# Kernel optimization log

Measured on AMD Instinct MI355X. Metric: run time of the kernel, lower is better.

Reference implementation:

```python
import jax, jax.numpy as jnp
import numpy as np

N_NODES = 100000
N_EDGES = 1600000
D_IN = 128
D_OUT = 128


def setup_inputs() -> dict:
    key = jax.random.key(0)
    ks = jax.random.split(key, 7)
    stdv = 1.0 / np.sqrt(D_OUT)
    x = jax.random.normal(ks[0], (N_NODES, D_IN), dtype=jnp.float32)
    W = jax.random.normal(ks[1], (D_IN, D_OUT), dtype=jnp.float32) * stdv
    lin_bias = jax.random.uniform(ks[2], (D_OUT,), minval=-stdv, maxval=stdv, dtype=jnp.float32)
    bias = jax.random.uniform(ks[3], (D_OUT,), minval=-stdv, maxval=stdv, dtype=jnp.float32)
    adj_rows = jax.random.randint(ks[4], (N_EDGES,), 0, N_NODES, dtype=jnp.int32)
    adj_cols = jax.random.randint(ks[5], (N_EDGES,), 0, N_NODES, dtype=jnp.int32)
    adj_vals = jax.random.uniform(ks[6], (N_EDGES,), dtype=jnp.float32)
    return {"x": x, "W": W, "lin_bias": lin_bias, "bias": bias,
            "adj_rows": adj_rows, "adj_cols": adj_cols, "adj_vals": adj_vals}


def reference(x, W, lin_bias, bias, adj_rows, adj_cols, adj_vals):
    # support = Linear(x)  -> [N, D_OUT]
    support = x @ W + lin_bias
    # out = spmm(adj, support): out[r] = sum_e vals[e] * support[cols[e]] for rows[e]==r
    msgs = adj_vals[:, None] * support[adj_cols]            # [E, D_OUT]
    out = jax.ops.segment_sum(msgs, adj_rows, num_segments=N_NODES)
    return out + bias
```

## Files before the change

### kernel.cpp

```cpp
#include <hip/hip_runtime.h>
#include <hip/hip_bf16.h>

#define N_NODES 100000
#define N_EDGES 1600000
#define D 128

#define NBLK 256
#define EPB (N_EDGES / NBLK)
#define BROWS 128
#define NB 782
#define PCAP 2816

typedef __attribute__((ext_vector_type(8))) short short8;
typedef __attribute__((ext_vector_type(4))) float f32x4;

__device__ inline unsigned short f2bf(float f) {
  union { float f; unsigned u; } c; c.f = f;
  const unsigned u = c.u;
  return (unsigned short)((u + 0x7FFF + ((u >> 16) & 1)) >> 16);
}
__device__ inline float bflo(unsigned u) { return __int_as_float(u << 16); }
__device__ inline float bfhi(unsigned u) { return __int_as_float(u & 0xFFFF0000u); }

__global__ __launch_bounds__(256) void prep_kernel(
    const float* __restrict__ W, unsigned short* __restrict__ Wt,
    int* __restrict__ gcur) {
  const int b = blockIdx.x;
  if (b < 16) {
    const int t = b * 256 + threadIdx.x;
    const int k = t >> 5, n4 = (t & 31) * 4;
    const float4 w = *(const float4*)(W + k * D + n4);
    Wt[(n4 + 0) * D + k] = f2bf(w.x);
    Wt[(n4 + 1) * D + k] = f2bf(w.y);
    Wt[(n4 + 2) * D + k] = f2bf(w.z);
    Wt[(n4 + 3) * D + k] = f2bf(w.w);
  } else {
    for (int i = threadIdx.x; i < NB; i += 256) gcur[i] = 0;
  }
}

#define GR 128
#define LDK 136
__global__ __launch_bounds__(256) void fused_kernel(
    const float* __restrict__ x, const unsigned short* __restrict__ Wt,
    const float* __restrict__ lin_bias, unsigned short* __restrict__ support,
    const int* __restrict__ rows, const int* __restrict__ cols,
    const float* __restrict__ vals, int* __restrict__ gcur,
    unsigned* __restrict__ pairs, unsigned char* __restrict__ rowlo) {
  __shared__ __align__(16) char smem[GR * LDK * 2];

  if (blockIdx.x < NBLK) {
    int* cnt = (int*)smem;
    int* cur = cnt + NB;
    const int t = threadIdx.x, blk = blockIdx.x;
    for (int i = t; i < NB; i += 256) cnt[i] = 0;
    __syncthreads();
    const int base = blk * EPB;
    for (int i = t; i < EPB; i += 256)
      atomicAdd(&cnt[rows[base + i] >> 7], 1);
    __syncthreads();
    for (int b = t; b < NB; b += 256) {
      const int c = cnt[b];
      cur[b] = c ? atomicAdd(&gcur[b], c) : 0;
    }
    __syncthreads();
    for (int i = t; i < EPB; i += 256) {
      const int e = base + i;
      const int r = rows[e];
      const int b = r >> 7;
      const int pos = atomicAdd(&cur[b], 1);
      if (pos < PCAP) {
        const unsigned q = (unsigned)(vals[e] * 32767.f + 0.5f);
        pairs[(size_t)b * PCAP + pos] = ((unsigned)cols[e] << 15) | q;
        rowlo[(size_t)b * PCAP + pos] = (unsigned char)(r & (BROWS - 1));
      }
    }
    return;
  }

  unsigned short* xb = (unsigned short*)smem;
  const int t = threadIdx.x;
  const int row0 = (blockIdx.x - NBLK) * GR;

  for (int i = t; i < GR * 32; i += 256) {
    const int r = i >> 5, k4 = (i & 31) * 4;
    const int row = row0 + r;
    float4 v = make_float4(0.f, 0.f, 0.f, 0.f);
    if (row < N_NODES) v = *(const float4*)(x + (size_t)row * D + k4);
    unsigned short* p = &xb[r * LDK + k4];
    p[0] = f2bf(v.x); p[1] = f2bf(v.y); p[2] = f2bf(v.z); p[3] = f2bf(v.w);
  }
  __syncthreads();

  const int w = t >> 6;
  const int lane = t & 63;
  const int m16 = lane & 15;
  const int quad = lane >> 4;

  f32x4 acc[2][8];
#pragma unroll
  for (int rt = 0; rt < 2; ++rt)
#pragma unroll
    for (int ct = 0; ct < 8; ++ct) acc[rt][ct] = (f32x4){0.f, 0.f, 0.f, 0.f};

#pragma unroll
  for (int kc = 0; kc < 4; ++kc) {
    const int kof = kc * 32 + quad * 8;
    short8 a0 = *(const short8*)&xb[(w * 32 + 0 * 16 + m16) * LDK + kof];
    short8 a1 = *(const short8*)&xb[(w * 32 + 1 * 16 + m16) * LDK + kof];
#pragma unroll
    for (int ct = 0; ct < 8; ++ct) {
      const short8 b = *(const short8*)&Wt[(size_t)(ct * 16 + m16) * D + kof];
      acc[0][ct] = __builtin_amdgcn_mfma_f32_16x16x32_bf16(a0, b, acc[0][ct], 0, 0, 0);
      acc[1][ct] = __builtin_amdgcn_mfma_f32_16x16x32_bf16(a1, b, acc[1][ct], 0, 0, 0);
    }
  }

#pragma unroll
  for (int ct = 0; ct < 8; ++ct) {
    const int col = ct * 16 + m16;
    const float lb = lin_bias[col];
#pragma unroll
    for (int rt = 0; rt < 2; ++rt) {
      const int rbase = row0 + w * 32 + rt * 16 + quad * 4;
#pragma unroll
      for (int i = 0; i < 4; ++i) {
        const int row = rbase + i;
        if (row < N_NODES)
          support[(size_t)row * D + col] = f2bf(acc[rt][ct][i] + lb);
      }
    }
  }
}

__global__ __launch_bounds__(512) void gather3_kernel(
    const int* __restrict__ gcur, const unsigned* __restrict__ pairs,
    const unsigned char* __restrict__ rowlo, const uint4* __restrict__ support,
    const float* __restrict__ bias, float* __restrict__ out) {
  __shared__ unsigned spair[PCAP];
  __shared__ unsigned char srl[PCAP];
  __shared__ unsigned short sidx[PCAP];
  __shared__ int rcnt[BROWS];
  __shared__ int rs[BROWS];
  __shared__ int rpos[BROWS];
  const int b = blockIdx.x, t = threadIdx.x;
  const int w = t >> 6, lane = t & 63;
  const int g = lane >> 4;
  const int c16 = lane & 15;
  const int r0 = b * BROWS;
  int m = gcur[b];
  if (m > PCAP) m = PCAP;
  const size_t pbase = (size_t)b * PCAP;

  for (int i = t; i < m; i += 512) {
    spair[i] = pairs[pbase + i];
    srl[i] = rowlo[pbase + i];
  }
  if (t < BROWS) rcnt[t] = 0;
  __syncthreads();
  for (int i = t; i < m; i += 512) atomicAdd(&rcnt[srl[i]], 1);
  __syncthreads();
  if (t < BROWS) rs[t] = rcnt[t];
  __syncthreads();
#pragma unroll
  for (int d = 1; d < BROWS; d <<= 1) {
    int v = 0;
    if (t < BROWS && t >= d) v = rs[t - d];
    __syncthreads();
    if (t < BROWS) rs[t] += v;
    __syncthreads();
  }
  if (t < BROWS) rpos[t] = rs[t] - rcnt[t];
  __syncthreads();
  for (int i = t; i < m; i += 512) {
    const int p = atomicAdd(&rpos[srl[i]], 1);
    sidx[p] = (unsigned short)i;
  }
  __syncthreads();

  for (int j = 0; j < 16; ++j) {
    const int rl = w * 16 + j;
    const int row = r0 + rl;
    if (row >= N_NODES) break;
    const int c = rcnt[rl];
    const int s = rs[rl] - c;

    float acc[8];
#pragma unroll
    for (int i = 0; i < 8; ++i) acc[i] = 0.f;

    for (int it = 0; it < c; it += 16) {
      const int ia = it + g;
      const int ib = it + 4 + g;
      const int ic = it + 8 + g;
      const int id = it + 12 + g;
      if (ia < c) {
        const unsigned p = spair[sidx[s + ia]];
        const float v = (float)(p & 0x7FFFu) * (1.f / 32767.f);
        const uint4 sv = support[(size_t)(p >> 15) * 16 + c16];
        acc[0] += v * bflo(sv.x); acc[1] += v * bfhi(sv.x);
        acc[2] += v * bflo(sv.y); acc[3] += v * bfhi(sv.y);
        acc[4] += v * bflo(sv.z); acc[5] += v * bfhi(sv.z);
        acc[6] += v * bflo(sv.w); acc[7] += v * bfhi(sv.w);
      }
      if (ib < c) {
        const unsigned p = spair[sidx[s + ib]];
        const float v = (float)(p & 0x7FFFu) * (1.f / 32767.f);
        const uint4 sv = support[(size_t)(p >> 15) * 16 + c16];
        acc[0] += v * bflo(sv.x); acc[1] += v * bfhi(sv.x);
        acc[2] += v * bflo(sv.y); acc[3] += v * bfhi(sv.y);
        acc[4] += v * bflo(sv.z); acc[5] += v * bfhi(sv.z);
        acc[6] += v * bflo(sv.w); acc[7] += v * bfhi(sv.w);
      }
      if (ic < c) {
        const unsigned p = spair[sidx[s + ic]];
        const float v = (float)(p & 0x7FFFu) * (1.f / 32767.f);
        const uint4 sv = support[(size_t)(p >> 15) * 16 + c16];
        acc[0] += v * bflo(sv.x); acc[1] += v * bfhi(sv.x);
        acc[2] += v * bflo(sv.y); acc[3] += v * bfhi(sv.y);
        acc[4] += v * bflo(sv.z); acc[5] += v * bfhi(sv.z);
        acc[6] += v * bflo(sv.w); acc[7] += v * bfhi(sv.w);
      }
      if (id < c) {
        const unsigned p = spair[sidx[s + id]];
        const float v = (float)(p & 0x7FFFu) * (1.f / 32767.f);
        const uint4 sv = support[(size_t)(p >> 15) * 16 + c16];
        acc[0] += v * bflo(sv.x); acc[1] += v * bfhi(sv.x);
        acc[2] += v * bflo(sv.y); acc[3] += v * bfhi(sv.y);
        acc[4] += v * bflo(sv.z); acc[5] += v * bfhi(sv.z);
        acc[6] += v * bflo(sv.w); acc[7] += v * bfhi(sv.w);
      }
    }

#pragma unroll
    for (int i = 0; i < 8; ++i) {
      acc[i] += __shfl_xor(acc[i], 16, 64);
      acc[i] += __shfl_xor(acc[i], 32, 64);
    }

    if (g == 0) {
      const float4 b0 = ((const float4*)bias)[c16 * 2 + 0];
      const float4 b1 = ((const float4*)bias)[c16 * 2 + 1];
      float4 o0, o1;
      o0.x = acc[0] + b0.x; o0.y = acc[1] + b0.y;
      o0.z = acc[2] + b0.z; o0.w = acc[3] + b0.w;
      o1.x = acc[4] + b1.x; o1.y = acc[5] + b1.y;
      o1.z = acc[6] + b1.z; o1.w = acc[7] + b1.w;
      float* op = out + (size_t)row * D + c16 * 8;
      *(float4*)(op + 0) = o0;
      *(float4*)(op + 4) = o1;
    }
  }
}

__global__ __launch_bounds__(256) void gemm_kernel(
    const float* __restrict__ x, const unsigned short* __restrict__ Wt,
    const float* __restrict__ lin_bias, unsigned short* __restrict__ support) {
  __shared__ unsigned short xb[GR * LDK];
  const int t = threadIdx.x;
  const int row0 = blockIdx.x * GR;

  for (int i = t; i < GR * 32; i += 256) {
    const int r = i >> 5, k4 = (i & 31) * 4;
    const int row = row0 + r;
    float4 v = make_float4(0.f, 0.f, 0.f, 0.f);
    if (row < N_NODES) v = *(const float4*)(x + (size_t)row * D + k4);
    unsigned short* p = &xb[r * LDK + k4];
    p[0] = f2bf(v.x); p[1] = f2bf(v.y); p[2] = f2bf(v.z); p[3] = f2bf(v.w);
  }
  __syncthreads();

  const int w = t >> 6;
  const int lane = t & 63;
  const int m16 = lane & 15;
  const int quad = lane >> 4;

  f32x4 acc[2][8];
#pragma unroll
  for (int rt = 0; rt < 2; ++rt)
#pragma unroll
    for (int ct = 0; ct < 8; ++ct) acc[rt][ct] = (f32x4){0.f, 0.f, 0.f, 0.f};

#pragma unroll
  for (int kc = 0; kc < 4; ++kc) {
    const int kof = kc * 32 + quad * 8;
    short8 a0 = *(const short8*)&xb[(w * 32 + 0 * 16 + m16) * LDK + kof];
    short8 a1 = *(const short8*)&xb[(w * 32 + 1 * 16 + m16) * LDK + kof];
#pragma unroll
    for (int ct = 0; ct < 8; ++ct) {
      const short8 b = *(const short8*)&Wt[(size_t)(ct * 16 + m16) * D + kof];
      acc[0][ct] = __builtin_amdgcn_mfma_f32_16x16x32_bf16(a0, b, acc[0][ct], 0, 0, 0);
      acc[1][ct] = __builtin_amdgcn_mfma_f32_16x16x32_bf16(a1, b, acc[1][ct], 0, 0, 0);
    }
  }

#pragma unroll
  for (int ct = 0; ct < 8; ++ct) {
    const int col = ct * 16 + m16;
    const float lb = lin_bias[col];
#pragma unroll
    for (int rt = 0; rt < 2; ++rt) {
      const int rbase = row0 + w * 32 + rt * 16 + quad * 4;
#pragma unroll
      for (int i = 0; i < 4; ++i) {
        const int row = rbase + i;
        if (row < N_NODES)
          support[(size_t)row * D + col] = f2bf(acc[rt][ct][i] + lb);
      }
    }
  }
}

__global__ __launch_bounds__(256) void init_out_kernel(
    const float* __restrict__ bias, float* __restrict__ out) {
  const size_t idx = (size_t)blockIdx.x * 256 + threadIdx.x;
  const float4 b = ((const float4*)bias)[idx & 31];
  ((float4*)out)[idx] = b;
}

__global__ __launch_bounds__(256) void scatter_kernel(
    const int* __restrict__ rows, const int* __restrict__ cols,
    const float* __restrict__ vals, const uint2* __restrict__ support,
    float* __restrict__ out) {
  const size_t tid = (size_t)blockIdx.x * 256 + threadIdx.x;
  const int e = (int)(tid >> 5);
  const int q = (int)(tid & 31);
  const int r = rows[e];
  const int c = cols[e];
  const float v = vals[e];
  const uint2 s = support[(size_t)c * 32 + q];
  float* o = out + (size_t)r * D + 4 * q;
  atomicAdd(o + 0, v * bflo(s.x));
  atomicAdd(o + 1, v * bfhi(s.x));
  atomicAdd(o + 2, v * bflo(s.y));
  atomicAdd(o + 3, v * bfhi(s.y));
}

extern "C" void kernel_launch(void* const* d_in, const int* in_sizes, int n_in,
                              void* d_out, int out_size, void* d_ws, size_t ws_size,
                              hipStream_t stream) {
  const float* x        = (const float*)d_in[0];
  const float* W        = (const float*)d_in[1];
  const float* lin_bias = (const float*)d_in[2];
  const float* bias     = (const float*)d_in[3];
  const int*   adj_rows = (const int*)d_in[4];
  const int*   adj_cols = (const int*)d_in[5];
  const float* adj_vals = (const float*)d_in[6];
  float* out = (float*)d_out;

  char* wsb = (char*)d_ws;
  unsigned short* support = (unsigned short*)wsb;
  unsigned*       pairs   = (unsigned*)(wsb + 25600000);
  unsigned char*  rowlo   = (unsigned char*)(wsb + 34408448);
  int*            gcur    = (int*)(wsb + 36610560);
  const size_t ws_needed = 36646464;

  const bool csr_path = (ws_size >= ws_needed);
  unsigned short* wt = (unsigned short*)(csr_path ? (wsb + 36613696)
                                                  : (wsb + 25600000));
  int* gcur_f = csr_path ? gcur : (int*)(wsb + 25600000 + 32768);

  prep_kernel<<<17, 256, 0, stream>>>(W, wt, gcur_f);

  if (csr_path) {
    fused_kernel<<<NBLK + (N_NODES + GR - 1) / GR, 256, 0, stream>>>(
        x, wt, lin_bias, support, adj_rows, adj_cols, adj_vals,
        gcur, pairs, rowlo);
    gather3_kernel<<<NB, 512, 0, stream>>>(gcur, pairs, rowlo,
                                           (const uint4*)support, bias, out);
  } else {
    gemm_kernel<<<(N_NODES + GR - 1) / GR, 256, 0, stream>>>(
        x, wt, lin_bias, support);
    init_out_kernel<<<12500, 256, 0, stream>>>(bias, out);
    scatter_kernel<<<200000, 256, 0, stream>>>(adj_rows, adj_cols, adj_vals,
                                               (const uint2*)support, out);
  }
}
```

Before: 263.9 us.

## Locally sort edges by bucket in shared memory before scattering pairs

Each binning block computes an exclusive scan of its per-bucket counts, stages edge indices and bucket ids in shared memory sorted by bucket, then writes pairs and row-low bytes in bucket order. Consecutive threads now write to contiguous global positions within a bucket instead of scattering at random. It adds a scan, an extra shared-memory pass and a re-read of rows, and uses nearly all of the shared buffer.

```diff
diff --git a/kernel.cpp b/kernel.cpp
--- a/kernel.cpp
+++ b/kernel.cpp
@@ -52,27 +52,71 @@
   if (blockIdx.x < NBLK) {
     int* cnt = (int*)smem;
     int* cur = cnt + NB;
+    int* gbase = cur + NB;
+    unsigned short* sidx = (unsigned short*)(gbase + NB);
+    unsigned short* sbkt = sidx + EPB;
+    int* wsum = (int*)(sbkt + EPB);
     const int t = threadIdx.x, blk = blockIdx.x;
+    const int w = t >> 6, lane = t & 63;
+    const int base = blk * EPB;
+
     for (int i = t; i < NB; i += 256) cnt[i] = 0;
     __syncthreads();
-    const int base = blk * EPB;
     for (int i = t; i < EPB; i += 256)
       atomicAdd(&cnt[rows[base + i] >> 7], 1);
     __syncthreads();
+
+    int s4[4]; int ssum = 0;
+#pragma unroll
+    for (int j = 0; j < 4; ++j) {
+      const int idx = t * 4 + j;
+      s4[j] = (idx < NB) ? cnt[idx] : 0;
+      ssum += s4[j];
+    }
+    int xi = ssum;
+#pragma unroll
+    for (int d = 1; d < 64; d <<= 1) {
+      const int y = __shfl_up(xi, d, 64);
+      if (lane >= d) xi += y;
+    }
+    if (lane == 63) wsum[w] = xi;
+    __syncthreads();
+    int pre = 0;
+#pragma unroll
+    for (int i = 0; i < 4; ++i) pre += (i < w) ? wsum[i] : 0;
+    int ex = pre + xi - ssum;
+#pragma unroll
+    for (int j = 0; j < 4; ++j) {
+      const int idx = t * 4 + j;
+      if (idx < NB) cur[idx] = ex;
+      ex += s4[j];
+    }
+    __syncthreads();
+
     for (int b = t; b < NB; b += 256) {
       const int c = cnt[b];
-      cur[b] = c ? atomicAdd(&gcur[b], c) : 0;
-    }
-    __syncthreads();
+      gbase[b] = c ? atomicAdd(&gcur[b], c) : 0;
+    }
+    __syncthreads();
+
     for (int i = t; i < EPB; i += 256) {
       const int e = base + i;
-      const int r = rows[e];
-      const int b = r >> 7;
-      const int pos = atomicAdd(&cur[b], 1);
-      if (pos < PCAP) {
+      const int b = rows[e] >> 7;
+      const int p = atomicAdd(&cur[b], 1);
+      sidx[p] = (unsigned short)i;
+      sbkt[p] = (unsigned short)b;
+    }
+    __syncthreads();
+
+    for (int p = t; p < EPB; p += 256) {
+      const int b = sbkt[p];
+      const int e = base + sidx[p];
+      const int lstart = cur[b] - cnt[b];
+      const int dst = gbase[b] + (p - lstart);
+      if (dst < PCAP) {
         const unsigned q = (unsigned)(vals[e] * 32767.f + 0.5f);
-        pairs[(size_t)b * PCAP + pos] = ((unsigned)cols[e] << 15) | q;
-        rowlo[(size_t)b * PCAP + pos] = (unsigned char)(r & (BROWS - 1));
+        pairs[(size_t)b * PCAP + dst] = ((unsigned)cols[e] << 15) | q;
+        rowlo[(size_t)b * PCAP + dst] = (unsigned char)(rows[e] & (BROWS - 1));
       }
     }
     return;
```

After: 247.2 us. -6.3%, faster.
